# Optimization experiments

Measured on AMD Instinct MI355X. Metric: run time of the kernel, lower is better.

The kernel has to match this reference:

```python
import jax, jax.numpy as jnp
import numpy as np

HEADS = 8
DIM_HEAD = 64
SCALE = DIM_HEAD ** -0.5

def layernorm_ch(x, g, eps=1e-5):
    # channel-wise LayerNorm over dim=1 (NCHW), biased variance
    mean = jnp.mean(x, axis=1, keepdims=True)
    var = jnp.var(x, axis=1, keepdims=True)
    return (x - mean) * jax.lax.rsqrt(var + eps) * g[None, :, None, None]

def setup_inputs() -> dict:
    key = jax.random.key(0)
    ks = jax.random.split(key, 4)
    B, C, H, W = 16, 512, 64, 64
    hidden = HEADS * DIM_HEAD
    x = jax.random.normal(ks[0], (B, C, H, W), dtype=jnp.float32)
    w_qkv = jax.random.normal(ks[1], (3 * hidden, C), dtype=jnp.float32) * (C ** -0.5)
    w_out = jax.random.normal(ks[2], (C, hidden), dtype=jnp.float32) * (hidden ** -0.5)
    b_out = jnp.zeros((C,), dtype=jnp.float32)
    g_out = jnp.ones((C,), dtype=jnp.float32)
    g_ln = jnp.ones((C,), dtype=jnp.float32)
    return {"x": x, "w_qkv": w_qkv, "w_out": w_out, "b_out": b_out, "g_out": g_out, "g_ln": g_ln}

def reference(x, w_qkv, w_out, b_out, g_out, g_ln):
    B, C, H, W = x.shape
    n = H * W
    x_norm = layernorm_ch(x, g_ln)
    # 1x1 conv == channel GEMM: [B,3*hidden,H,W]
    qkv = jnp.einsum('oc,bchw->bohw', w_qkv, x_norm)
    q, k, v = jnp.split(qkv, 3, axis=1)
    # b (h d) x y -> b h d n
    def to_heads(t):
        return t.reshape(B, HEADS, DIM_HEAD, n)
    q, k, v = to_heads(q), to_heads(k), to_heads(v)
    q = jax.nn.softmax(q, axis=-2) * SCALE   # softmax over d
    k = jax.nn.softmax(k, axis=-1)           # softmax over n
    v = v / n
    context = jnp.einsum('bhdn,bhen->bhde', k, v)
    out = jnp.einsum('bhde,bhdn->bhen', context, q)
    out = out.reshape(B, HEADS * DIM_HEAD, H, W)
    out = jnp.einsum('oc,bchw->bohw', w_out, out) + b_out[None, :, None, None]
    out = layernorm_ch(out, g_out)
    return out + x
```

## Files before the change

### kernel.cpp

```cpp
#include <hip/hip_runtime.h>
#include <math.h>

#define CCH    512
#define HWN    4096
#define NPIX   65536
#define OC3    1536
#define QSCALE 0.125f
#define LN_EPS 1e-5f

typedef _Float16 h16;
typedef h16  f16x8 __attribute__((ext_vector_type(8)));
typedef float f32x4 __attribute__((ext_vector_type(4)));

__device__ __forceinline__ float waveReduceSum(float v) {
#pragma unroll
    for (int off = 32; off; off >>= 1) v += __shfl_xor(v, off);
    return v;
}

__device__ __forceinline__ void gl_lds16(const void* g, void* l) {
    __builtin_amdgcn_global_load_lds((const __attribute__((address_space(1))) void*)g,
                                     (__attribute__((address_space(3))) void*)l, 16, 0, 0);
}

__global__ __launch_bounds__(64) void prep_w(const float* __restrict__ w_qkv,
                                             const float* __restrict__ g_ln,
                                             const float* __restrict__ w_out,
                                             h16* __restrict__ wg_h,
                                             float* __restrict__ s,
                                             h16* __restrict__ wo_h) {
    const int o = blockIdx.x, lane = threadIdx.x;
    if (o < OC3) {
        float sum = 0.f;
#pragma unroll
        for (int j = 0; j < 8; ++j) {
            const int c = lane + j * 64;
            const float w = w_qkv[(size_t)o * CCH + c] * g_ln[c];
            wg_h[(size_t)o * CCH + c] = (h16)(w * 64.f);
            sum += w;
        }
        sum = waveReduceSum(sum);
        if (lane == 0) s[o] = sum;
    } else {
        const int r = o - OC3;
#pragma unroll
        for (int j = 0; j < 8; ++j) {
            const int c = lane + j * 64;
            wo_h[(size_t)r * CCH + c] = (h16)(w_out[(size_t)r * CCH + c] * 64.f);
        }
    }
}

__global__ __launch_bounds__(256) void transpose_cvt(const float* __restrict__ src,
                                                     h16* __restrict__ dhi,
                                                     float* __restrict__ psum,
                                                     float* __restrict__ psq) {
    __shared__ float tile[64][65];
    __shared__ float ps1[4][64], ps2[4][64];
    const int b = blockIdx.z, c0 = blockIdx.y * 64, p0 = blockIdx.x * 64;
    const int t = threadIdx.x;
    const float* sb = src + ((size_t)b * CCH + c0) * HWN + p0;
    const int rc = t >> 4, cc4 = (t & 15) * 4;
#pragma unroll
    for (int ps = 0; ps < 4; ++ps) {
        const float4 v = *(const float4*)(sb + (size_t)(rc + ps * 16) * HWN + cc4);
        tile[rc + ps * 16][cc4 + 0] = v.x;
        tile[rc + ps * 16][cc4 + 1] = v.y;
        tile[rc + ps * 16][cc4 + 2] = v.z;
        tile[rc + ps * 16][cc4 + 3] = v.w;
    }
    __syncthreads();
    {
        const int q = t >> 6, px = t & 63;
        float s1 = 0.f, s2 = 0.f;
#pragma unroll
        for (int c = q * 16; c < q * 16 + 16; ++c) {
            const float v = tile[c][px];
            s1 += v; s2 += v * v;
        }
        ps1[q][px] = s1; ps2[q][px] = s2;
    }
    const int pr0 = t >> 3, cs = (t & 7) * 8;
#pragma unroll
    for (int ps = 0; ps < 2; ++ps) {
        const int pr = pr0 + ps * 32;
        f16x8 vh;
#pragma unroll
        for (int q = 0; q < 8; ++q) vh[q] = (h16)tile[cs + q][pr];
        const size_t o = ((size_t)b * HWN + p0 + pr) * CCH + c0 + cs;
        *(f16x8*)(dhi + o) = vh;
    }
    __syncthreads();
    if (t < 64) {
        const float s1 = ps1[0][t] + ps1[1][t] + ps1[2][t] + ps1[3][t];
        const float s2 = ps2[0][t] + ps2[1][t] + ps2[2][t] + ps2[3][t];
        const size_t gp = (size_t)b * HWN + p0 + t;
        psum[(size_t)(c0 >> 6) * NPIX + gp] = s1;
        psq [(size_t)(c0 >> 6) * NPIX + gp] = s2;
    }
}

__global__ __launch_bounds__(512) void qkv_gemm(const h16* __restrict__ Ahg,
                                                const h16* __restrict__ Bhg,
                                                const float* __restrict__ sv,
                                                const float* __restrict__ psum,
                                                const float* __restrict__ psq,
                                                h16* __restrict__ qout) {
    __shared__ __align__(16) h16 Ah[8192];
    __shared__ __align__(16) h16 Bh[16384];
    __shared__ float mnS[256], rsS[256];
    const int tid = threadIdx.x;
    const int om = blockIdx.x * 128;
    const int by0 = blockIdx.y;
    const int by  = (by0 & 7) * 32 + (by0 >> 3);
    const int p0  = by * 256;

    const int srow = tid >> 2;
    const int skh  = ((tid & 3) ^ (srow & 3)) * 8;
    const size_t a0 = (size_t)(om + srow) * CCH + skh;
    const size_t b0 = (size_t)(p0 + srow) * CCH + skh;

    const int lane = tid & 63;
    const int wv = tid >> 6;
    const int wm = (wv >> 2) * 64, wn = (wv & 3) * 64;
    const int lr = lane & 15, kg = lane >> 4;
    const int swz = (kg ^ (lr & 3)) * 8;

    f32x4 acc[4][4];
#pragma unroll
    for (int i = 0; i < 4; ++i)
#pragma unroll
        for (int j = 0; j < 4; ++j) acc[i][j] = {0.f, 0.f, 0.f, 0.f};

#define STAGE(KC)                                                          \
    do {                                                                   \
        gl_lds16(Ahg + a0 + (KC),                 Ah + tid * 8);           \
        gl_lds16(Ahg + a0 + (KC) + 32,            Ah + 4096 + tid * 8);    \
        gl_lds16(Bhg + b0 + (KC),                 Bh + tid * 8);           \
        gl_lds16(Bhg + b0 + (KC) + 128 * CCH,     Bh + 4096 + tid * 8);    \
        gl_lds16(Bhg + b0 + (KC) + 32,            Bh + 8192 + tid * 8);    \
        gl_lds16(Bhg + b0 + (KC) + 32 + 128 * CCH, Bh + 12288 + tid * 8);  \
    } while (0)

    STAGE(0);
    if (tid < 256) {
        const int gp = p0 + tid;
        float s1 = 0.f, s2 = 0.f;
#pragma unroll
        for (int cb = 0; cb < 8; ++cb) {
            s1 += psum[(size_t)cb * NPIX + gp];
            s2 += psq [(size_t)cb * NPIX + gp];
        }
        const float m = s1 * (1.f / 512.f);
        float var = s2 * (1.f / 512.f) - m * m;
        var = fmaxf(var, 0.f);
        mnS[tid] = m;
        rsS[tid] = rsqrtf(var + LN_EPS);
    }

#pragma unroll 1
    for (int kc = 0; kc < 512; kc += 64) {
        __syncthreads();
        f16x8 a0f[4], b0f[4], a1f[4], b1f[4];
#pragma unroll
        for (int i = 0; i < 4; ++i) {
            a0f[i] = *(const f16x8*)(Ah + (wm + i * 16 + lr) * 32 + swz);
            b0f[i] = *(const f16x8*)(Bh + (wn + i * 16 + lr) * 32 + swz);
        }
#pragma unroll
        for (int i = 0; i < 4; ++i)
#pragma unroll
            for (int j = 0; j < 4; ++j)
                acc[i][j] = __builtin_amdgcn_mfma_f32_16x16x32_f16(a0f[i], b0f[j], acc[i][j], 0, 0, 0);
#pragma unroll
        for (int i = 0; i < 4; ++i) {
            a1f[i] = *(const f16x8*)(Ah + 4096 + (wm + i * 16 + lr) * 32 + swz);
            b1f[i] = *(const f16x8*)(Bh + 8192 + (wn + i * 16 + lr) * 32 + swz);
        }
        __syncthreads();
        if (kc + 64 < 512) STAGE(kc + 64);
#pragma unroll
        for (int i = 0; i < 4; ++i)
#pragma unroll
            for (int j = 0; j < 4; ++j)
                acc[i][j] = __builtin_amdgcn_mfma_f32_16x16x32_f16(a1f[i], b1f[j], acc[i][j], 0, 0, 0);
    }
#undef STAGE

    const int b = p0 >> 12, hw0 = p0 & 4095;
    float mn[4], rs[4];
#pragma unroll
    for (int j = 0; j < 4; ++j) {
        const int px = wn + j * 16 + lr;
        mn[j] = mnS[px]; rs[j] = rsS[px];
    }
#pragma unroll
    for (int i = 0; i < 4; ++i)
#pragma unroll
        for (int r = 0; r < 4; ++r) {
            const int o = om + wm + i * 16 + kg * 4 + r;
            const float so = sv[o];
            h16* dst = qout + ((size_t)b * OC3 + o) * HWN;
#pragma unroll
            for (int j = 0; j < 4; ++j) {
                const int hw = hw0 + wn + j * 16 + lr;
                dst[hw] = (h16)(rs[j] * (acc[i][j][r] * (1.f / 64.f) - mn[j] * so));
            }
        }
}

__global__ __launch_bounds__(256) void ctx_partial(const h16* __restrict__ qkv16,
                                                   float* __restrict__ ctp) {
    __shared__ float kt[64][68];
    __shared__ float vt[64][68];

    const int bh = blockIdx.y, ci = blockIdx.x;
    const int b = bh >> 3, h = bh & 7;
    const h16* kb = qkv16 + ((size_t)b * OC3 + CCH  + h * 64) * HWN;
    const h16* vb = qkv16 + ((size_t)b * OC3 + 1024 + h * 64) * HWN;
    const int tid = threadIdx.x;

    const int d  = tid >> 2;
    const int td = tid & 15, te = tid >> 4;

    float mx = -1e30f;
    for (int t = 0; t < 8; ++t) {
        const int n0 = ci * 512 + t * 64;
#pragma unroll
        for (int jj = 0; jj < 2; ++jj) {
            const int nn = (tid & 3) * 8 + jj * 32;
            const f16x8 kv = *(const f16x8*)(kb + (size_t)d * HWN + n0 + nn);
#pragma unroll
            for (int u = 0; u < 8; ++u) mx = fmaxf(mx, (float)kv[u]);
        }
    }
    mx = fmaxf(mx, __shfl_xor(mx, 1));
    mx = fmaxf(mx, __shfl_xor(mx, 2));

    float zt = 0.f;
    float acc[4][4];
#pragma unroll
    for (int i = 0; i < 4; ++i)
#pragma unroll
        for (int j = 0; j < 4; ++j) acc[i][j] = 0.f;

    for (int t = 0; t < 8; ++t) {
        const int n0 = ci * 512 + t * 64;
        __syncthreads();
#pragma unroll
        for (int jj = 0; jj < 2; ++jj) {
            const int nn = (tid & 3) * 8 + jj * 32;
            const f16x8 kv = *(const f16x8*)(kb + (size_t)d * HWN + n0 + nn);
            const f16x8 vv = *(const f16x8*)(vb + (size_t)d * HWN + n0 + nn);
#pragma unroll
            for (int u = 0; u < 8; ++u) {
                const float e = __expf((float)kv[u] - mx);
                zt += e;
                kt[nn + u][d] = e;
                vt[nn + u][d] = (float)vv[u];
            }
        }
        __syncthreads();
#pragma unroll
        for (int nn = 0; nn < 64; ++nn) {
            float kf[4], vf[4];
            *(float4*)kf = *(const float4*)&kt[nn][td * 4];
            *(float4*)vf = *(const float4*)&vt[nn][te * 4];
#pragma unroll
            for (int i = 0; i < 4; ++i)
#pragma unroll
                for (int j = 0; j < 4; ++j)
                    acc[i][j] = fmaf(kf[i], vf[j], acc[i][j]);
        }
    }
    zt += __shfl_xor(zt, 1);
    zt += __shfl_xor(zt, 2);

    float* dst = ctp + ((size_t)bh * 8 + ci) * 4224;
#pragma unroll
    for (int i = 0; i < 4; ++i) {
        const float4 o4 = make_float4(acc[i][0], acc[i][1], acc[i][2], acc[i][3]);
        *(float4*)(dst + (td * 4 + i) * 64 + te * 4) = o4;
    }
    if ((tid & 3) == 0) {
        dst[4096 + d] = zt;
        dst[4160 + d] = mx;
    }
}

__global__ __launch_bounds__(256) void ctx_reduce(const float* __restrict__ ctp,
                                                  float* __restrict__ ct) {
    __shared__ float w[8][64];
    __shared__ float rz[64];
    const int bh = blockIdx.x;
    const int tid = threadIdx.x;
    const float* src = ctp + (size_t)bh * 8 * 4224;
    if (tid < 64) {
        float M = -1e30f;
#pragma unroll
        for (int ci = 0; ci < 8; ++ci)
            M = fmaxf(M, src[(size_t)ci * 4224 + 4160 + tid]);
        float Z = 0.f;
#pragma unroll
        for (int ci = 0; ci < 8; ++ci) {
            const float ww = __expf(src[(size_t)ci * 4224 + 4160 + tid] - M);
            w[ci][tid] = ww;
            Z += ww * src[(size_t)ci * 4224 + 4096 + tid];
        }
        rz[tid] = 1.f / Z;
    }
    __syncthreads();
    float* dst = ct + (size_t)bh * 4096;
    for (int e4 = tid * 4; e4 < 4096; e4 += 1024) {
        const int d = e4 >> 6;
        float4 sum = make_float4(0.f, 0.f, 0.f, 0.f);
#pragma unroll
        for (int ci = 0; ci < 8; ++ci) {
            const float4 v = *(const float4*)(src + (size_t)ci * 4224 + e4);
            const float ww = w[ci][d];
            sum.x += ww * v.x; sum.y += ww * v.y;
            sum.z += ww * v.z; sum.w += ww * v.w;
        }
        const float r = rz[d];
        sum.x *= r; sum.y *= r; sum.z *= r; sum.w *= r;
        *(float4*)(dst + e4) = sum;
    }
}

__global__ __launch_bounds__(256) void attn_out(const h16* __restrict__ qkv16,
                                                const float* __restrict__ ct,
                                                h16* __restrict__ at) {
    __shared__ float cts[64][68];
    __shared__ float qt[64][68];

    const int bh = blockIdx.y, ci = blockIdx.x;
    const int b = bh >> 3, h = bh & 7;
    const h16* qb = qkv16 + ((size_t)b * OC3 + h * 64) * HWN;
    const int tid = threadIdx.x;

    for (int i4 = tid * 4; i4 < 4096; i4 += 1024) {
        const float4 v = *(const float4*)(ct + (size_t)bh * 4096 + i4);
        *(float4*)&cts[i4 >> 6][i4 & 63] = v;
    }

    const int d  = tid >> 2;
    const int te = tid & 15, tn = tid >> 4;
    const int rn = tid >> 2, d0q = (tid & 3) * 16;

    for (int t = 0; t < 8; ++t) {
        const int n0 = ci * 512 + t * 64;
        __syncthreads();
#pragma unroll
        for (int jj = 0; jj < 2; ++jj) {
            const int nn = (tid & 3) * 8 + jj * 32;
            const f16x8 qv = *(const f16x8*)(qb + (size_t)d * HWN + n0 + nn);
#pragma unroll
            for (int u = 0; u < 8; ++u) qt[nn + u][d] = (float)qv[u];
        }
        __syncthreads();
        {
            float mx = -1e30f;
#pragma unroll
            for (int dd = 0; dd < 16; ++dd) mx = fmaxf(mx, qt[rn][d0q + dd]);
            mx = fmaxf(mx, __shfl_xor(mx, 1));
            mx = fmaxf(mx, __shfl_xor(mx, 2));
            float sm = 0.f;
#pragma unroll
            for (int dd = 0; dd < 16; ++dd) sm += __expf(qt[rn][d0q + dd] - mx);
            sm += __shfl_xor(sm, 1);
            sm += __shfl_xor(sm, 2);
            const float sc = 512.f * QSCALE / sm;
#pragma unroll
            for (int dd = 0; dd < 16; ++dd)
                qt[rn][d0q + dd] = __expf(qt[rn][d0q + dd] - mx) * sc;
        }
        __syncthreads();
        float acc[4][4];
#pragma unroll
        for (int i = 0; i < 4; ++i)
#pragma unroll
            for (int j = 0; j < 4; ++j) acc[i][j] = 0.f;
#pragma unroll
        for (int dd = 0; dd < 64; ++dd) {
            float cv[4];
            *(float4*)cv = *(const float4*)&cts[dd][te * 4];
            const float q0 = qt[tn * 4 + 0][dd];
            const float q1 = qt[tn * 4 + 1][dd];
            const float q2 = qt[tn * 4 + 2][dd];
            const float q3 = qt[tn * 4 + 3][dd];
#pragma unroll
            for (int i = 0; i < 4; ++i) {
                acc[i][0] = fmaf(cv[i], q0, acc[i][0]);
                acc[i][1] = fmaf(cv[i], q1, acc[i][1]);
                acc[i][2] = fmaf(cv[i], q2, acc[i][2]);
                acc[i][3] = fmaf(cv[i], q3, acc[i][3]);
            }
        }
        __syncthreads();
#pragma unroll
        for (int i = 0; i < 4; ++i)
#pragma unroll
            for (int j = 0; j < 4; ++j)
                qt[tn * 4 + j][te * 4 + i] = acc[i][j];
        __syncthreads();
        {
            const int px = tid >> 2, e0 = (tid & 3) * 16;
            f16x8 vh0, vh1;
#pragma unroll
            for (int u = 0; u < 8; ++u) {
                vh0[u] = (h16)qt[px][e0 + u];
                vh1[u] = (h16)qt[px][e0 + 8 + u];
            }
            const size_t o = ((size_t)b * HWN + n0 + px) * CCH + h * 64 + e0;
            *(f16x8*)(at + o)     = vh0;
            *(f16x8*)(at + o + 8) = vh1;
        }
    }
}

__global__ __launch_bounds__(512) void out_fused(const h16* __restrict__ wo_hi,
                                                 const h16* __restrict__ at,
                                                 const float* __restrict__ b_out,
                                                 const float* __restrict__ g_out,
                                                 const float* __restrict__ x,
                                                 float* __restrict__ out) {
    __shared__ __align__(16) h16 Alds[512 * 32];
    __shared__ __align__(16) h16 Blds[128 * 32];
    __shared__ float red1[4][128], red2[4][128];
    __shared__ float mnS[128], rsS[128];

    const int tid = threadIdx.x;
    const int p0 = blockIdx.x * 128;
    const int b = p0 >> 12, hw0 = p0 & 4095;

    const int trow = tid >> 2;
    const int skh  = ((tid & 3) ^ (trow & 3)) * 8;
    const size_t aoff = (size_t)trow * CCH + skh;
    const size_t boff = (size_t)p0 * CCH + aoff;
    const int wofs = (tid >> 6) * 512;

    const int wv = tid >> 6;
    const int wm = (wv >> 1) * 128, wn = (wv & 1) * 64;
    const int lane = tid & 63;
    const int lr = lane & 15, kg = lane >> 4;
    const int swz = (kg ^ (lr & 3)) * 8;

    f32x4 acc[8][4];
#pragma unroll
    for (int i = 0; i < 8; ++i)
#pragma unroll
        for (int j = 0; j < 4; ++j) acc[i][j] = {0.f, 0.f, 0.f, 0.f};

#define STAGEF(S)                                                           \
    do {                                                                    \
        const int kc_ = (S) * 32;                                           \
        gl_lds16(wo_hi + aoff + kc_,               Alds + wofs);            \
        gl_lds16(wo_hi + aoff + kc_ + 128 * CCH,   Alds + 4096 + wofs);     \
        gl_lds16(wo_hi + aoff + kc_ + 256 * CCH,   Alds + 8192 + wofs);     \
        gl_lds16(wo_hi + aoff + kc_ + 384 * CCH,   Alds + 12288 + wofs);    \
        gl_lds16(at + boff + kc_,                  Blds + wofs);            \
    } while (0)

    STAGEF(0);
#pragma unroll 1
    for (int s = 0; s < 16; ++s) {
        __syncthreads();
        f16x8 af[8], bf[4];
#pragma unroll
        for (int i = 0; i < 8; ++i)
            af[i] = *(const f16x8*)(Alds + (wm + i * 16 + lr) * 32 + swz);
#pragma unroll
        for (int j = 0; j < 4; ++j)
            bf[j] = *(const f16x8*)(Blds + (wn + j * 16 + lr) * 32 + swz);
        __syncthreads();
        if (s < 15) STAGEF(s + 1);
#pragma unroll
        for (int i = 0; i < 8; ++i)
#pragma unroll
            for (int j = 0; j < 4; ++j)
                acc[i][j] = __builtin_amdgcn_mfma_f32_16x16x32_f16(af[i], bf[j], acc[i][j], 0, 0, 0);
    }
#undef STAGEF

#pragma unroll
    for (int i = 0; i < 8; ++i) {
        const int o = wm + i * 16 + kg * 4;
        const float4 bb = *(const float4*)(b_out + o);
#pragma unroll
        for (int j = 0; j < 4; ++j) {
            acc[i][j][0] = acc[i][j][0] * (1.f / 134217728.f) + bb.x;
            acc[i][j][1] = acc[i][j][1] * (1.f / 134217728.f) + bb.y;
            acc[i][j][2] = acc[i][j][2] * (1.f / 134217728.f) + bb.z;
            acc[i][j][3] = acc[i][j][3] * (1.f / 134217728.f) + bb.w;
        }
    }
    float s1[4], s2[4];
#pragma unroll
    for (int j = 0; j < 4; ++j) {
        s1[j] = 0.f; s2[j] = 0.f;
#pragma unroll
        for (int i = 0; i < 8; ++i)
#pragma unroll
            for (int r = 0; r < 4; ++r) {
                const float v = acc[i][j][r];
                s1[j] += v; s2[j] += v * v;
            }
        s1[j] += __shfl_xor(s1[j], 16); s1[j] += __shfl_xor(s1[j], 32);
        s2[j] += __shfl_xor(s2[j], 16); s2[j] += __shfl_xor(s2[j], 32);
    }
    if (kg == 0) {
#pragma unroll
        for (int j = 0; j < 4; ++j) {
            red1[wv >> 1][wn + j * 16 + lr] = s1[j];
            red2[wv >> 1][wn + j * 16 + lr] = s2[j];
        }
    }
    __syncthreads();
    if (tid < 128) {
        const float S1 = red1[0][tid] + red1[1][tid] + red1[2][tid] + red1[3][tid];
        const float S2 = red2[0][tid] + red2[1][tid] + red2[2][tid] + red2[3][tid];
        const float m = S1 * (1.f / 512.f);
        float var = S2 * (1.f / 512.f) - m * m;
        var = fmaxf(var, 0.f);
        mnS[tid] = m;
        rsS[tid] = rsqrtf(var + LN_EPS);
    }
    __syncthreads();
    float mj[4], rj[4];
#pragma unroll
    for (int j = 0; j < 4; ++j) {
        const int px = wn + j * 16 + lr;
        mj[j] = mnS[px]; rj[j] = rsS[px];
    }
#pragma unroll
    for (int i = 0; i < 8; ++i) {
        const int o = wm + i * 16 + kg * 4;
        const float4 gg = *(const float4*)(g_out + o);
#pragma unroll
        for (int r = 0; r < 4; ++r) {
            const float g = (r == 0) ? gg.x : (r == 1) ? gg.y : (r == 2) ? gg.z : gg.w;
            const float* xr = x + ((size_t)b * CCH + o + r) * HWN + hw0 + wn;
            float* dr = out + ((size_t)b * CCH + o + r) * HWN + hw0 + wn;
#pragma unroll
            for (int j = 0; j < 4; ++j) {
                const int c = j * 16 + lr;
                dr[c] = (acc[i][j][r] - mj[j]) * rj[j] * g + xr[c];
            }
        }
    }
}

extern "C" void kernel_launch(void* const* d_in, const int* in_sizes, int n_in,
                              void* d_out, int out_size, void* d_ws, size_t ws_size,
                              hipStream_t stream) {
    (void)in_sizes; (void)n_in; (void)out_size;
    const float* x     = (const float*)d_in[0];
    const float* w_qkv = (const float*)d_in[1];
    const float* w_out = (const float*)d_in[2];
    const float* b_out = (const float*)d_in[3];
    const float* g_out = (const float*)d_in[4];
    const float* g_ln  = (const float*)d_in[5];
    float* out = (float*)d_out;
    float* ws  = (float*)d_ws;

    float* s    = ws;
    float* ct   = s + OC3;
    float* ctp  = ct + 524288;
    float* psum = ctp;
    float* psq  = psum + 524288;
    h16*  wg_hi = (h16*)(ctp + 4325376);
    h16*  wo_hi = wg_hi + 786432;
    h16*  qkv16 = wo_hi + 262144;
    h16*  at    = qkv16 + 100663296;
    h16*  xt_hi = (h16*)d_out;

    const size_t need = 72484352ULL * 4ULL;
    if (ws_size < need) return;

    prep_w       <<<2048, 64, 0, stream>>>(w_qkv, g_ln, w_out, wg_hi, s, wo_hi);
    transpose_cvt<<<dim3(64, 8, 16), 256, 0, stream>>>(x, xt_hi, psum, psq);
    qkv_gemm     <<<dim3(12, 256), 512, 0, stream>>>(wg_hi, xt_hi,
                                                     s, psum, psq, qkv16);
    ctx_partial  <<<dim3(8, 128), 256, 0, stream>>>(qkv16, ctp);
    ctx_reduce   <<<128, 256, 0, stream>>>(ctp, ct);
    attn_out     <<<dim3(8, 128), 256, 0, stream>>>(qkv16, ct, at);
    out_fused    <<<512, 512, 0, stream>>>(wo_hi, at,
                                           b_out, g_out, x, out);
}
```

Measured before the change: 452.5 us.

## Compute K-context with MFMA and fuse K row-max into QKV GEMM epilogue

The QKV GEMM epilogue now computes per-64-pixel row maxima of K and writes them to a new workspace buffer. ctx_partial drops its separate max pass and its LDS-staged scalar FMA loop. Instead it forms exp(k-m) in fp16 registers and accumulates K·Vᵀ with 16x16x32 f16 MFMA in single-wave blocks over 16 chunks, and ctx_reduce now merges 16 partials. This removes a redundant K read and moves the context GEMM onto matrix cores, at the cost of storing the exponentials in fp16 (lower precision) and extra shuffles in the GEMM epilogue.

```diff
diff --git a/kernel.cpp b/kernel.cpp
--- a/kernel.cpp
+++ b/kernel.cpp
@@ -105,7 +105,8 @@
                                                 const float* __restrict__ sv,
                                                 const float* __restrict__ psum,
                                                 const float* __restrict__ psq,
-                                                h16* __restrict__ qout) {
+                                                h16* __restrict__ qout,
+                                                float* __restrict__ km) {
     __shared__ __align__(16) h16 Ah[8192];
     __shared__ __align__(16) h16 Bh[16384];
     __shared__ float mnS[256], rsS[256];
@@ -188,6 +189,7 @@
 #undef STAGE
 
     const int b = p0 >> 12, hw0 = p0 & 4095;
+    const bool isK = (blockIdx.x >= 4 && blockIdx.x < 8);
     float mn[4], rs[4];
 #pragma unroll
     for (int j = 0; j < 4; ++j) {
@@ -201,108 +203,110 @@
             const int o = om + wm + i * 16 + kg * 4 + r;
             const float so = sv[o];
             h16* dst = qout + ((size_t)b * OC3 + o) * HWN;
+            float mx = -1e30f;
 #pragma unroll
             for (int j = 0; j < 4; ++j) {
                 const int hw = hw0 + wn + j * 16 + lr;
-                dst[hw] = (h16)(rs[j] * (acc[i][j][r] * (1.f / 64.f) - mn[j] * so));
-            }
-        }
-}
-
-__global__ __launch_bounds__(256) void ctx_partial(const h16* __restrict__ qkv16,
-                                                   float* __restrict__ ctp) {
-    __shared__ float kt[64][68];
-    __shared__ float vt[64][68];
-
+                const float val = rs[j] * (acc[i][j][r] * (1.f / 64.f) - mn[j] * so);
+                dst[hw] = (h16)val;
+                mx = fmaxf(mx, val);
+            }
+            if (isK) {
+                mx = fmaxf(mx, __shfl_xor(mx, 1));
+                mx = fmaxf(mx, __shfl_xor(mx, 2));
+                mx = fmaxf(mx, __shfl_xor(mx, 4));
+                mx = fmaxf(mx, __shfl_xor(mx, 8));
+                if (lr == 0)
+                    km[(size_t)(b * 512 + (o - CCH)) * 64 + (p0 >> 6) + (wn >> 6)] = mx;
+            }
+        }
+}
+
+__global__ __launch_bounds__(64) void ctx_partial(const h16* __restrict__ qkv16,
+                                                  const float* __restrict__ km,
+                                                  float* __restrict__ ctp) {
     const int bh = blockIdx.y, ci = blockIdx.x;
     const int b = bh >> 3, h = bh & 7;
     const h16* kb = qkv16 + ((size_t)b * OC3 + CCH  + h * 64) * HWN;
     const h16* vb = qkv16 + ((size_t)b * OC3 + 1024 + h * 64) * HWN;
-    const int tid = threadIdx.x;
-
-    const int d  = tid >> 2;
-    const int td = tid & 15, te = tid >> 4;
-
-    float mx = -1e30f;
-    for (int t = 0; t < 8; ++t) {
-        const int n0 = ci * 512 + t * 64;
-#pragma unroll
-        for (int jj = 0; jj < 2; ++jj) {
-            const int nn = (tid & 3) * 8 + jj * 32;
-            const f16x8 kv = *(const f16x8*)(kb + (size_t)d * HWN + n0 + nn);
-#pragma unroll
-            for (int u = 0; u < 8; ++u) mx = fmaxf(mx, (float)kv[u]);
-        }
-    }
-    mx = fmaxf(mx, __shfl_xor(mx, 1));
-    mx = fmaxf(mx, __shfl_xor(mx, 2));
-
-    float zt = 0.f;
-    float acc[4][4];
+    const int lane = threadIdx.x;
+    const int lr = lane & 15, kg = lane >> 4;
+
+    float m[4];
+#pragma unroll
+    for (int i = 0; i < 4; ++i) {
+        const float* kmr = km + ((size_t)bh * 64 + i * 16 + lr) * 64 + ci * 4;
+        m[i] = fmaxf(fmaxf(kmr[0], kmr[1]), fmaxf(kmr[2], kmr[3]));
+    }
+    float z[4] = {0.f, 0.f, 0.f, 0.f};
+    f32x4 acc[4][4];
 #pragma unroll
     for (int i = 0; i < 4; ++i)
 #pragma unroll
-        for (int j = 0; j < 4; ++j) acc[i][j] = 0.f;
-
-    for (int t = 0; t < 8; ++t) {
-        const int n0 = ci * 512 + t * 64;
-        __syncthreads();
-#pragma unroll
-        for (int jj = 0; jj < 2; ++jj) {
-            const int nn = (tid & 3) * 8 + jj * 32;
-            const f16x8 kv = *(const f16x8*)(kb + (size_t)d * HWN + n0 + nn);
-            const f16x8 vv = *(const f16x8*)(vb + (size_t)d * HWN + n0 + nn);
+        for (int j = 0; j < 4; ++j) acc[i][j] = {0.f, 0.f, 0.f, 0.f};
+
+    const int nbase = ci * 256 + kg * 8;
+#pragma unroll 1
+    for (int c = 0; c < 8; ++c) {
+        const int n0 = nbase + c * 32;
+        f16x8 ke[4], vf[4];
+#pragma unroll
+        for (int j = 0; j < 4; ++j)
+            vf[j] = *(const f16x8*)(vb + (size_t)(j * 16 + lr) * HWN + n0);
+#pragma unroll
+        for (int i = 0; i < 4; ++i) {
+            const f16x8 kv = *(const f16x8*)(kb + (size_t)(i * 16 + lr) * HWN + n0);
+            f16x8 t;
 #pragma unroll
             for (int u = 0; u < 8; ++u) {
-                const float e = __expf((float)kv[u] - mx);
-                zt += e;
-                kt[nn + u][d] = e;
-                vt[nn + u][d] = (float)vv[u];
-            }
-        }
-        __syncthreads();
-#pragma unroll
-        for (int nn = 0; nn < 64; ++nn) {
-            float kf[4], vf[4];
-            *(float4*)kf = *(const float4*)&kt[nn][td * 4];
-            *(float4*)vf = *(const float4*)&vt[nn][te * 4];
-#pragma unroll
-            for (int i = 0; i < 4; ++i)
-#pragma unroll
-                for (int j = 0; j < 4; ++j)
-                    acc[i][j] = fmaf(kf[i], vf[j], acc[i][j]);
-        }
-    }
-    zt += __shfl_xor(zt, 1);
-    zt += __shfl_xor(zt, 2);
-
-    float* dst = ctp + ((size_t)bh * 8 + ci) * 4224;
+                const float e = __expf((float)kv[u] - m[i]);
+                z[i] += e;
+                t[u] = (h16)e;
+            }
+            ke[i] = t;
+        }
+#pragma unroll
+        for (int i = 0; i < 4; ++i)
+#pragma unroll
+            for (int j = 0; j < 4; ++j)
+                acc[i][j] = __builtin_amdgcn_mfma_f32_16x16x32_f16(ke[i], vf[j], acc[i][j], 0, 0, 0);
+    }
 #pragma unroll
     for (int i = 0; i < 4; ++i) {
-        const float4 o4 = make_float4(acc[i][0], acc[i][1], acc[i][2], acc[i][3]);
-        *(float4*)(dst + (td * 4 + i) * 64 + te * 4) = o4;
-    }
-    if ((tid & 3) == 0) {
-        dst[4096 + d] = zt;
-        dst[4160 + d] = mx;
-    }
+        z[i] += __shfl_xor(z[i], 16);
+        z[i] += __shfl_xor(z[i], 32);
+    }
+    float* dst = ctp + ((size_t)bh * 16 + ci) * 4224;
+#pragma unroll
+    for (int i = 0; i < 4; ++i)
+#pragma unroll
+        for (int j = 0; j < 4; ++j)
+#pragma unroll
+            for (int r = 0; r < 4; ++r)
+                dst[(i * 16 + kg * 4 + r) * 64 + j * 16 + lr] = acc[i][j][r];
+    if (kg == 0)
+#pragma unroll
+        for (int i = 0; i < 4; ++i) {
+            dst[4096 + i * 16 + lr] = z[i];
+            dst[4160 + i * 16 + lr] = m[i];
+        }
 }
 
 __global__ __launch_bounds__(256) void ctx_reduce(const float* __restrict__ ctp,
                                                   float* __restrict__ ct) {
-    __shared__ float w[8][64];
+    __shared__ float w[16][64];
     __shared__ float rz[64];
     const int bh = blockIdx.x;
     const int tid = threadIdx.x;
-    const float* src = ctp + (size_t)bh * 8 * 4224;
+    const float* src = ctp + (size_t)bh * 16 * 4224;
     if (tid < 64) {
         float M = -1e30f;
 #pragma unroll
-        for (int ci = 0; ci < 8; ++ci)
+        for (int ci = 0; ci < 16; ++ci)
             M = fmaxf(M, src[(size_t)ci * 4224 + 4160 + tid]);
         float Z = 0.f;
 #pragma unroll
-        for (int ci = 0; ci < 8; ++ci) {
+        for (int ci = 0; ci < 16; ++ci) {
             const float ww = __expf(src[(size_t)ci * 4224 + 4160 + tid] - M);
             w[ci][tid] = ww;
             Z += ww * src[(size_t)ci * 4224 + 4096 + tid];
@@ -315,7 +319,7 @@
         const int d = e4 >> 6;
         float4 sum = make_float4(0.f, 0.f, 0.f, 0.f);
 #pragma unroll
-        for (int ci = 0; ci < 8; ++ci) {
+        for (int ci = 0; ci < 16; ++ci) {
             const float4 v = *(const float4*)(src + (size_t)ci * 4224 + e4);
             const float ww = w[ci][d];
             sum.x += ww * v.x; sum.y += ww * v.y;
@@ -565,23 +569,24 @@
 
     float* s    = ws;
     float* ct   = s + OC3;
-    float* ctp  = ct + 524288;
+    float* km   = ct + 524288;
+    float* ctp  = km + 524288;
     float* psum = ctp;
     float* psq  = psum + 524288;
-    h16*  wg_hi = (h16*)(ctp + 4325376);
+    h16*  wg_hi = (h16*)(ctp + 8650752);
     h16*  wo_hi = wg_hi + 786432;
     h16*  qkv16 = wo_hi + 262144;
     h16*  at    = qkv16 + 100663296;
     h16*  xt_hi = (h16*)d_out;
 
-    const size_t need = 72484352ULL * 4ULL;
+    const size_t need = 77334016ULL * 4ULL;
     if (ws_size < need) return;
 
     prep_w       <<<2048, 64, 0, stream>>>(w_qkv, g_ln, w_out, wg_hi, s, wo_hi);
     transpose_cvt<<<dim3(64, 8, 16), 256, 0, stream>>>(x, xt_hi, psum, psq);
     qkv_gemm     <<<dim3(12, 256), 512, 0, stream>>>(wg_hi, xt_hi,
-                                                     s, psum, psq, qkv16);
-    ctx_partial  <<<dim3(8, 128), 256, 0, stream>>>(qkv16, ctp);
+                                                     s, psum, psq, qkv16, km);
+    ctx_partial  <<<dim3(16, 128), 64, 0, stream>>>(qkv16, km, ctp);
     ctx_reduce   <<<128, 256, 0, stream>>>(ctp, ct);
     attn_out     <<<dim3(8, 128), 256, 0, stream>>>(qkv16, ct, at);
     out_fused    <<<512, 512, 0, stream>>>(wo_hi, at,
```

Measured after the change: 442.5 us. 1.02x faster.
